# Kernel optimization log

Measured on AMD Instinct MI355X. Metric: run time of the kernel, lower is better.

Reference implementation:

```python
import jax, jax.numpy as jnp
import numpy as np

B, C, H, W = 4, 192, 128, 128
K = 4                       # cross-scan directions (all identical tokens since L=1, but distinct weights)
DSTATE = 8
DTRANK = max(8, C // 16)    # 12
EPS = 1e-5


def _ln(x, w, b):
    mu = jnp.mean(x, axis=-1, keepdims=True)
    var = jnp.var(x, axis=-1, keepdims=True)
    return (x - mu) * jax.lax.rsqrt(var + EPS) * w + b


def setup_inputs() -> dict:
    key = jax.random.key(0)
    ks = jax.random.split(key, 16)
    s_in = 1.0 / np.sqrt(C)
    inp = {
        "x": jax.random.normal(ks[0], (B, C, H, W), jnp.float32),
        "norm_w": 1.0 + 0.02 * jax.random.normal(ks[1], (C,), jnp.float32),
        "norm_b": 0.02 * jax.random.normal(ks[2], (C,), jnp.float32),
        "w_in": s_in * jax.random.normal(ks[3], (2 * C, C), jnp.float32),
        "ssm_in_w": s_in * jax.random.normal(ks[4], (2 * C, C), jnp.float32),
        "x_proj_w": s_in * jax.random.normal(ks[5], (K, DTRANK + 2 * DSTATE, C), jnp.float32),
        "dt_w": (1.0 / np.sqrt(DTRANK)) * jax.random.normal(ks[6], (K, C, DTRANK), jnp.float32),
        "dt_b": 0.1 * jax.random.normal(ks[7], (K, C), jnp.float32),
        "A_logs": jnp.log(jnp.broadcast_to(jnp.arange(1, DSTATE + 1, dtype=jnp.float32), (K * C, DSTATE))),
        "Ds": jnp.ones((K * C,), jnp.float32),
        "out_norm_w": 1.0 + 0.02 * jax.random.normal(ks[8], (C,), jnp.float32),
        "out_norm_b": 0.02 * jax.random.normal(ks[9], (C,), jnp.float32),
        "ssm_out_w": s_in * jax.random.normal(ks[10], (C, C), jnp.float32),
        "w_out": s_in * jax.random.normal(ks[11], (C, C), jnp.float32),
    }
    return inp


def reference(x, norm_w, norm_b, w_in, ssm_in_w, x_proj_w, dt_w, dt_b,
              A_logs, Ds, out_norm_w, out_norm_b, ssm_out_w, w_out):
    # (B,C,H,W) -> (B,H,W,C)
    xh = jnp.transpose(x, (0, 2, 3, 1))
    xn = _ln(xh, norm_w, norm_b)
    p = xn @ w_in.T                         # (B,H,W,2C)
    x1, x2 = p[..., :C], p[..., C:]

    # ---- SS2D (v2, d_conv=1) on per-pixel sequences of length 1 ----
    u = x1 @ ssm_in_w.T                     # (B,H,W,2C)
    xss, z = u[..., :C], u[..., C:]
    z = jax.nn.silu(z)
    xss = jax.nn.silu(xss)

    # x_proj per direction: (B,H,W,K,dt_rank+2*d_state)
    xd = jnp.einsum('bhwd,kcd->bhwkc', xss, x_proj_w)
    dtr = xd[..., :DTRANK]
    Bv = xd[..., DTRANK:DTRANK + DSTATE]
    Cv = xd[..., DTRANK + DSTATE:]
    dt = jax.nn.softplus(jnp.einsum('bhwkr,kdr->bhwkd', dtr, dt_w) + dt_b)

    # Selective scan with L=1 and h0=0: h = dt*B*xss; y_k = sum_s C_s*h_s + D*xss
    # => y = xss * sum_k ( (B . C)_k * dt_k + D_k ).  A = -exp(A_logs) never enters (L=1).
    bc = jnp.sum(Bv * Cv, axis=-1)          # (B,H,W,K)
    gain = jnp.sum(bc[..., None] * dt + Ds.reshape(K, C), axis=-2)  # (B,H,W,C)
    y = xss * gain
    y = _ln(y, out_norm_w, out_norm_b)
    y = y * z
    s = y @ ssm_out_w.T                     # SS2D out_proj

    # ---- block gating + out_proj + residual ----
    o = (s * jax.nn.silu(x2)) @ w_out.T
    return x + jnp.transpose(o, (0, 3, 1, 2))
```

## Files before the change

kernel.cpp:

```cpp
#include <hip/hip_runtime.h>
#include <hip/hip_bf16.h>
#include <math.h>


#define CC    192
#define HH    128
#define WW    128
#define NK    4
#define DST   8
#define DTR   12
#define TP    32
#define SP    200
#define NTH   256

typedef __attribute__((ext_vector_type(8))) short bh8;
typedef __attribute__((ext_vector_type(4))) float f4;

#define OFF_WIN    0
#define OFF_SSMIN  73728
#define OFF_XPROJ  147456
#define OFF_SSMOUT 168960
#define OFF_WOUT   205824
#define OFF_DTW    242688
#define WTOT2      267264

__device__ __forceinline__ float bf2f(unsigned short u) {
    union { unsigned int i; float f; } v; v.i = ((unsigned int)u) << 16; return v.f;
}
__device__ __forceinline__ unsigned short f2bf(float f) {
    union { float f; unsigned int i; } v; v.f = f;
    unsigned int r = (v.i + 0x7fffu + ((v.i >> 16) & 1u)) >> 16;
    return (unsigned short)r;
}
#define LOG2E 1.44269504f
#define LN2   0.69314718f
__device__ __forceinline__ float silu_fast(float x) {
    float e = __builtin_amdgcn_exp2f(-LOG2E * x);
    return x * __builtin_amdgcn_rcpf(1.f + e);
}
__device__ __forceinline__ float softplus_fast(float x) {
    float e = __builtin_amdgcn_exp2f(-LOG2E * fabsf(x));
    return fmaxf(x, 0.f) + LN2 * __builtin_amdgcn_logf(1.f + e);
}

extern "C" __global__ void prep_w(const float* __restrict__ w_in,
                                  const float* __restrict__ ssm_in_w,
                                  const float* __restrict__ x_proj_w,
                                  const float* __restrict__ ssm_out_w,
                                  const float* __restrict__ w_out,
                                  const float* __restrict__ dt_w,
                                  const float* __restrict__ dt_b,
                                  const float* __restrict__ Ds,
                                  unsigned short* __restrict__ wb)
{
    int i = blockIdx.x * NTH + threadIdx.x;
    if (i < OFF_DTW) {
        float v;
        if      (i < OFF_XPROJ ) v = (i < OFF_SSMIN) ? w_in[i] : ssm_in_w[i - OFF_SSMIN];
        else if (i < OFF_SSMOUT) v = x_proj_w[i - OFF_XPROJ];
        else if (i < OFF_WOUT  ) v = ssm_out_w[i - OFF_SSMOUT];
        else                     v = w_out[i - OFF_WOUT];
        wb[i] = f2bf(v);
    } else if (i < WTOT2) {
        int j  = i - OFF_DTW;
        int r  = j & 31;
        int kc = j >> 5;
        float v = (r < DTR) ? dt_w[kc * DTR + r]
                            : (r == 31 ? dt_b[kc] : 0.f);
        wb[i] = f2bf(v);
    } else if (i < WTOT2 + CC) {
        int c = i - WTOT2;
        float* dsum = (float*)(wb + WTOT2);
        dsum[c] = Ds[c] + Ds[CC + c] + Ds[2*CC + c] + Ds[3*CC + c];
    }
}

extern "C" __global__ void __launch_bounds__(NTH, 3)
mamba_fused(const float* __restrict__ x,
            const float* __restrict__ norm_w,  const float* __restrict__ norm_b,
            const float* __restrict__ out_norm_w, const float* __restrict__ out_norm_b,
            const unsigned short* __restrict__ wsb,
            float* __restrict__ out)
{
    __shared__ __align__(16) unsigned short sA [TP][SP];
    __shared__ __align__(16) unsigned short sB [TP][SP];
    __shared__ __align__(16) unsigned short sZ [TP][CC];
    __shared__ __align__(16) unsigned short sX2[TP][CC];
    __shared__ float sred [TP][8];
    __shared__ float sred2[TP][8];
    __shared__ float smu[TP];
    __shared__ float srs[TP];
    __shared__ __align__(16) float sbcT[NK][TP];

    const int tid  = threadIdx.x;
    const int lane = tid & 63;
    const int wave = tid >> 6;
    const int frow = lane & 15;
    const int kb   = lane >> 4;
    const int pxb  = kb * 4;

    const int t   = blockIdx.x;
    const int b   = t >> 9;
    const int rem = t & 511;
    const int h   = rem >> 2;
    const int w0g = (rem & 3) * TP;

    const float* dsum = (const float*)(wsb + WTOT2);

    {
        const int px = tid & 31, part = tid >> 5;
        float sum = 0.f, sq = 0.f;
        const size_t base = (((size_t)b * CC) * HH + h) * WW + w0g + px;
        for (int i = 0; i < 24; ++i) {
            int c = part * 24 + i;
            float v = x[base + (size_t)c * (HH * WW)];
            sum += v; sq += v * v;
            sA[px][c] = f2bf(v);
        }
        sred[px][part] = sum; sred2[px][part] = sq;
        __syncthreads();
        if (part == 0) {
            float s = 0.f, q = 0.f;
            for (int j = 0; j < 8; ++j) { s += sred[px][j]; q += sred2[px][j]; }
            float mu  = s * (1.f / CC);
            float var = q * (1.f / CC) - mu * mu;
            smu[px] = mu; srs[px] = rsqrtf(var + 1e-5f);
        }
        __syncthreads();
        const float mu = smu[px], rs = srs[px];
        for (int i = 0; i < 24; ++i) {
            int c = part * 24 + i;
            float v = bf2f(sA[px][c]);
            v = (v - mu) * rs * norm_w[c] + norm_b[c];
            sA[px][c] = f2bf(v);
        }
        __syncthreads();
    }

    auto load_a = [&](const unsigned short* sSrc, bh8 a[2][6]) {
#pragma unroll
        for (int m = 0; m < 2; ++m)
#pragma unroll
            for (int ks = 0; ks < 6; ++ks)
                a[m][ks] = *(const bh8*)(sSrc + (m * 16 + frow) * SP + ks * 32 + kb * 8);
    };
    auto gemm_nt = [&](const bh8 a[2][6], const unsigned short* wB, int n0,
                       f4& acc0, f4& acc1) {
        const unsigned short* wp = wB + (size_t)(n0 + frow) * CC + kb * 8;
#pragma unroll
        for (int ks = 0; ks < 6; ++ks) {
            bh8 bf = *(const bh8*)(wp + ks * 32);
            acc0 = __builtin_amdgcn_mfma_f32_16x16x32_bf16(a[0][ks], bf, acc0, 0, 0, 0);
            acc1 = __builtin_amdgcn_mfma_f32_16x16x32_bf16(a[1][ks], bf, acc1, 0, 0, 0);
        }
    };

    {
        bh8 a[2][6]; load_a(&sA[0][0], a);
        const unsigned short* wB = wsb + OFF_WIN;
        for (int nt = wave; nt < 24; nt += 4) {
            f4 acc0 = {0.f,0.f,0.f,0.f}, acc1 = {0.f,0.f,0.f,0.f};
            gemm_nt(a, wB, nt * 16, acc0, acc1);
            int o = nt * 16 + frow;
            if (o < CC) {
#pragma unroll
                for (int r = 0; r < 4; ++r) {
                    sB[pxb + r][o]      = f2bf(acc0[r]);
                    sB[16 + pxb + r][o] = f2bf(acc1[r]);
                }
            } else {
                int oc = o - CC;
#pragma unroll
                for (int r = 0; r < 4; ++r) {
                    sX2[pxb + r][oc]      = f2bf(silu_fast(acc0[r]));
                    sX2[16 + pxb + r][oc] = f2bf(silu_fast(acc1[r]));
                }
            }
        }
    }
    __syncthreads();

    {
        bh8 a[2][6]; load_a(&sB[0][0], a);
        const unsigned short* wB = wsb + OFF_SSMIN;
        for (int nt = wave; nt < 24; nt += 4) {
            f4 acc0 = {0.f,0.f,0.f,0.f}, acc1 = {0.f,0.f,0.f,0.f};
            gemm_nt(a, wB, nt * 16, acc0, acc1);
            int o = nt * 16 + frow;
            if (o < CC) {
#pragma unroll
                for (int r = 0; r < 4; ++r) {
                    sA[pxb + r][o]      = f2bf(silu_fast(acc0[r]));
                    sA[16 + pxb + r][o] = f2bf(silu_fast(acc1[r]));
                }
            } else {
                int oc = o - CC;
#pragma unroll
                for (int r = 0; r < 4; ++r) {
                    sZ[pxb + r][oc]      = f2bf(silu_fast(acc0[r]));
                    sZ[16 + pxb + r][oc] = f2bf(silu_fast(acc1[r]));
                }
            }
        }
    }
    __syncthreads();

    {
        bh8 a[2][6]; load_a(&sA[0][0], a);
        const unsigned short* wB = wsb + OFF_XPROJ;
        for (int nt = wave; nt < 7; nt += 4) {
            f4 acc0 = {0.f,0.f,0.f,0.f}, acc1 = {0.f,0.f,0.f,0.f};
            gemm_nt(a, wB, nt * 16, acc0, acc1);
            int o = nt * 16 + frow;
#pragma unroll
            for (int r = 0; r < 4; ++r) {
                sB[pxb + r][o]      = f2bf(acc0[r]);
                sB[16 + pxb + r][o] = f2bf(acc1[r]);
            }
        }
    }
    __syncthreads();

    if (tid < TP * NK) {
        int px = tid & 31, k = tid >> 5;
        float a = 0.f;
        for (int s = 0; s < DST; ++s)
            a += bf2f(sB[px][k*28 + DTR + s]) * bf2f(sB[px][k*28 + DTR + DST + s]);
        sbcT[k][px] = a;
    }
    __syncthreads();

    {
        bh8 adt[NK][2];
#pragma unroll
        for (int k = 0; k < NK; ++k)
#pragma unroll
            for (int m = 0; m < 2; ++m) {
                const unsigned short* rp = &sB[m * 16 + frow][k * 28];
                bh8 v;
                if (kb == 0) {
                    ushort4 lo = *(const ushort4*)(rp);
                    ushort4 hi = *(const ushort4*)(rp + 4);
                    v = bh8{(short)lo.x,(short)lo.y,(short)lo.z,(short)lo.w,
                            (short)hi.x,(short)hi.y,(short)hi.z,(short)hi.w};
                } else if (kb == 1) {
                    ushort4 lo = *(const ushort4*)(rp + 8);
                    v = bh8{(short)lo.x,(short)lo.y,(short)lo.z,(short)lo.w,0,0,0,0};
                } else if (kb == 2) {
                    v = bh8{0,0,0,0,0,0,0,0};
                } else {
                    v = bh8{0,0,0,0,0,0,0,(short)0x3F80};
                }
                adt[k][m] = v;
            }
        f4 bc0[NK], bc1[NK];
#pragma unroll
        for (int k = 0; k < NK; ++k) {
            bc0[k] = *(const f4*)(&sbcT[k][pxb]);
            bc1[k] = *(const f4*)(&sbcT[k][16 + pxb]);
        }
        const unsigned short* wDT = wsb + OFF_DTW;
        for (int ct = wave; ct < 12; ct += 4) {
            int c = ct * 16 + frow;
            f4 g0 = {0.f,0.f,0.f,0.f}, g1 = {0.f,0.f,0.f,0.f};
#pragma unroll
            for (int k = 0; k < NK; ++k) {
                bh8 bf = *(const bh8*)(wDT + (((size_t)(k * CC + c)) << 5) + kb * 8);
                f4 d0 = {0.f,0.f,0.f,0.f}, d1 = {0.f,0.f,0.f,0.f};
                d0 = __builtin_amdgcn_mfma_f32_16x16x32_bf16(adt[k][0], bf, d0, 0, 0, 0);
                d1 = __builtin_amdgcn_mfma_f32_16x16x32_bf16(adt[k][1], bf, d1, 0, 0, 0);
#pragma unroll
                for (int r = 0; r < 4; ++r) {
                    g0[r] += bc0[k][r] * softplus_fast(d0[r]);
                    g1[r] += bc1[k][r] * softplus_fast(d1[r]);
                }
            }
            float ds = dsum[c];
#pragma unroll
            for (int r = 0; r < 4; ++r) {
                float y0 = bf2f(sA[pxb + r][c]) * (g0[r] + ds);
                sA[pxb + r][c] = f2bf(y0);
                float y1 = bf2f(sA[16 + pxb + r][c]) * (g1[r] + ds);
                sA[16 + pxb + r][c] = f2bf(y1);
            }
        }
    }
    __syncthreads();

    {
        const int px = tid & 31, part = tid >> 5;
        float sum = 0.f, sq = 0.f;
        for (int i = 0; i < 24; ++i) {
            int c = part * 24 + i;
            float v = bf2f(sA[px][c]);
            sum += v; sq += v * v;
        }
        sred[px][part] = sum; sred2[px][part] = sq;
        __syncthreads();
        if (part == 0) {
            float s = 0.f, q = 0.f;
            for (int j = 0; j < 8; ++j) { s += sred[px][j]; q += sred2[px][j]; }
            float mu  = s * (1.f / CC);
            float var = q * (1.f / CC) - mu * mu;
            smu[px] = mu; srs[px] = rsqrtf(var + 1e-5f);
        }
        __syncthreads();
        const float mu = smu[px], rs = srs[px];
        for (int i = 0; i < 24; ++i) {
            int c = part * 24 + i;
            float v = bf2f(sA[px][c]);
            v = (v - mu) * rs * out_norm_w[c] + out_norm_b[c];
            v *= bf2f(sZ[px][c]);
            sA[px][c] = f2bf(v);
        }
        __syncthreads();
    }

    {
        bh8 a[2][6]; load_a(&sA[0][0], a);
        const unsigned short* wB = wsb + OFF_SSMOUT;
        for (int nt = wave; nt < 12; nt += 4) {
            f4 acc0 = {0.f,0.f,0.f,0.f}, acc1 = {0.f,0.f,0.f,0.f};
            gemm_nt(a, wB, nt * 16, acc0, acc1);
            int o = nt * 16 + frow;
#pragma unroll
            for (int r = 0; r < 4; ++r) {
                sB[pxb + r][o]      = f2bf(acc0[r] * bf2f(sX2[pxb + r][o]));
                sB[16 + pxb + r][o] = f2bf(acc1[r] * bf2f(sX2[16 + pxb + r][o]));
            }
        }
    }
    __syncthreads();

    {
        bh8 a[2][6]; load_a(&sB[0][0], a);
        const unsigned short* wB = wsb + OFF_WOUT;
        for (int nt = wave; nt < 12; nt += 4) {
            f4 acc0 = {0.f,0.f,0.f,0.f}, acc1 = {0.f,0.f,0.f,0.f};
            gemm_nt(a, wB, nt * 16, acc0, acc1);
            int o = nt * 16 + frow;
            const size_t g0 = (((size_t)b * CC + o) * HH + h) * WW + w0g;
#pragma unroll
            for (int r = 0; r < 4; ++r) {
                out[g0 + pxb + r]      = x[g0 + pxb + r]      + acc0[r];
                out[g0 + 16 + pxb + r] = x[g0 + 16 + pxb + r] + acc1[r];
            }
        }
    }
}

extern "C" void kernel_launch(void* const* d_in, const int* in_sizes, int n_in,
                              void* d_out, int out_size, void* d_ws, size_t ws_size,
                              hipStream_t stream) {
    const float* x          = (const float*)d_in[0];
    const float* norm_w     = (const float*)d_in[1];
    const float* norm_b     = (const float*)d_in[2];
    const float* w_in       = (const float*)d_in[3];
    const float* ssm_in_w   = (const float*)d_in[4];
    const float* x_proj_w   = (const float*)d_in[5];
    const float* dt_w       = (const float*)d_in[6];
    const float* dt_b       = (const float*)d_in[7];
    const float* Ds         = (const float*)d_in[9];
    const float* out_norm_w = (const float*)d_in[10];
    const float* out_norm_b = (const float*)d_in[11];
    const float* ssm_out_w  = (const float*)d_in[12];
    const float* w_out      = (const float*)d_in[13];

    unsigned short* wb = (unsigned short*)d_ws;
    int prep_n = WTOT2 + CC;
    prep_w<<<dim3((prep_n + NTH - 1) / NTH), dim3(NTH), 0, stream>>>(
        w_in, ssm_in_w, x_proj_w, ssm_out_w, w_out, dt_w, dt_b, Ds, wb);

    mamba_fused<<<dim3(2048), dim3(NTH), 0, stream>>>(
        x, norm_w, norm_b, out_norm_w, out_norm_b, wb, (float*)d_out);
}
```

Measured before the change: 176.3 us.

## Keep x2 gate in registers, pair MFMA tiles, raise occupancy to 4 blocks

The silu(x2) gate is now packed as bf16 pairs and held in registers across stages instead of in a shared-memory sX2 buffer. This removes about 12 KB of LDS per block, and the launch bound is raised from 3 to 4 blocks per CU to use the freed space. The GEMM loops are unrolled into explicit pairs of 16-wide output tiles so each wave issues four independent MFMA chains per k-step, giving more instruction-level parallelism. Other tweaks: bf16 conversion now uses the HIP intrinsic, and the bc loads are moved inside the dt loop to cut register pressure. The risk is VGPR spilling under the tighter 4-block bound, and the x_proj stage now computes an extra padded tile.

```diff
diff --git a/kernel.cpp b/kernel.cpp
--- a/kernel.cpp
+++ b/kernel.cpp
@@ -24,14 +24,21 @@
 #define OFF_DTW    242688
 #define WTOT2      267264
 
+#define MFMA(va, vb, vc) __builtin_amdgcn_mfma_f32_16x16x32_bf16(va, vb, vc, 0, 0, 0)
+
 __device__ __forceinline__ float bf2f(unsigned short u) {
     union { unsigned int i; float f; } v; v.i = ((unsigned int)u) << 16; return v.f;
 }
 __device__ __forceinline__ unsigned short f2bf(float f) {
-    union { float f; unsigned int i; } v; v.f = f;
-    unsigned int r = (v.i + 0x7fffu + ((v.i >> 16) & 1u)) >> 16;
-    return (unsigned short)r;
-}
+    __hip_bfloat16 h = __float2bfloat16(f);
+    unsigned short u; __builtin_memcpy(&u, &h, 2); return u;
+}
+__device__ __forceinline__ unsigned int pk2(float a, float b) {
+    return (unsigned int)f2bf(a) | ((unsigned int)f2bf(b) << 16);
+}
+__device__ __forceinline__ float lo16(unsigned int u) { return bf2f((unsigned short)(u & 0xffffu)); }
+__device__ __forceinline__ float hi16(unsigned int u) { return bf2f((unsigned short)(u >> 16)); }
+
 #define LOG2E 1.44269504f
 #define LN2   0.69314718f
 __device__ __forceinline__ float silu_fast(float x) {
@@ -75,7 +82,7 @@
     }
 }
 
-extern "C" __global__ void __launch_bounds__(NTH, 3)
+extern "C" __global__ void __launch_bounds__(NTH, 4)
 mamba_fused(const float* __restrict__ x,
             const float* __restrict__ norm_w,  const float* __restrict__ norm_b,
             const float* __restrict__ out_norm_w, const float* __restrict__ out_norm_b,
@@ -85,7 +92,6 @@
     __shared__ __align__(16) unsigned short sA [TP][SP];
     __shared__ __align__(16) unsigned short sB [TP][SP];
     __shared__ __align__(16) unsigned short sZ [TP][CC];
-    __shared__ __align__(16) unsigned short sX2[TP][CC];
     __shared__ float sred [TP][8];
     __shared__ float sred2[TP][8];
     __shared__ float smu[TP];
@@ -106,6 +112,8 @@
     const int w0g = (rem & 3) * TP;
 
     const float* dsum = (const float*)(wsb + WTOT2);
+
+    uint2 x2a0, x2a1, x2a2, x2b0, x2b1, x2b2;
 
     {
         const int px = tid & 31, part = tid >> 5;
@@ -144,38 +152,76 @@
             for (int ks = 0; ks < 6; ++ks)
                 a[m][ks] = *(const bh8*)(sSrc + (m * 16 + frow) * SP + ks * 32 + kb * 8);
     };
-    auto gemm_nt = [&](const bh8 a[2][6], const unsigned short* wB, int n0,
-                       f4& acc0, f4& acc1) {
+    auto gemm_pair = [&](const bh8 a[2][6], const unsigned short* wB, int n0, int n1,
+                         f4& p0, f4& p1, f4& q0, f4& q1) {
+        const unsigned short* wp0 = wB + (size_t)(n0 + frow) * CC + kb * 8;
+        const unsigned short* wp1 = wB + (size_t)(n1 + frow) * CC + kb * 8;
+#pragma unroll
+        for (int ks = 0; ks < 6; ++ks) {
+            bh8 b0 = *(const bh8*)(wp0 + ks * 32);
+            bh8 b1 = *(const bh8*)(wp1 + ks * 32);
+            p0 = MFMA(a[0][ks], b0, p0);
+            p1 = MFMA(a[1][ks], b0, p1);
+            q0 = MFMA(a[0][ks], b1, q0);
+            q1 = MFMA(a[1][ks], b1, q1);
+        }
+    };
+    auto gemm_one = [&](const bh8 a[2][6], const unsigned short* wB, int n0,
+                        f4& p0, f4& p1) {
         const unsigned short* wp = wB + (size_t)(n0 + frow) * CC + kb * 8;
 #pragma unroll
         for (int ks = 0; ks < 6; ++ks) {
             bh8 bf = *(const bh8*)(wp + ks * 32);
-            acc0 = __builtin_amdgcn_mfma_f32_16x16x32_bf16(a[0][ks], bf, acc0, 0, 0, 0);
-            acc1 = __builtin_amdgcn_mfma_f32_16x16x32_bf16(a[1][ks], bf, acc1, 0, 0, 0);
-        }
+            p0 = MFMA(a[0][ks], bf, p0);
+            p1 = MFMA(a[1][ks], bf, p1);
+        }
+    };
+    auto st_sB = [&](int o, const f4& c0, const f4& c1) {
+#pragma unroll
+        for (int r = 0; r < 4; ++r) {
+            sB[pxb + r][o]      = f2bf(c0[r]);
+            sB[16 + pxb + r][o] = f2bf(c1[r]);
+        }
+    };
+    auto st_sA_silu = [&](int o, const f4& c0, const f4& c1) {
+#pragma unroll
+        for (int r = 0; r < 4; ++r) {
+            sA[pxb + r][o]      = f2bf(silu_fast(c0[r]));
+            sA[16 + pxb + r][o] = f2bf(silu_fast(c1[r]));
+        }
+    };
+    auto st_sZ_silu = [&](int oc, const f4& c0, const f4& c1) {
+#pragma unroll
+        for (int r = 0; r < 4; ++r) {
+            sZ[pxb + r][oc]      = f2bf(silu_fast(c0[r]));
+            sZ[16 + pxb + r][oc] = f2bf(silu_fast(c1[r]));
+        }
+    };
+    auto pack_silu = [&](const f4& c) {
+        return make_uint2(pk2(silu_fast(c[0]), silu_fast(c[1])),
+                          pk2(silu_fast(c[2]), silu_fast(c[3])));
     };
 
     {
         bh8 a[2][6]; load_a(&sA[0][0], a);
         const unsigned short* wB = wsb + OFF_WIN;
-        for (int nt = wave; nt < 24; nt += 4) {
-            f4 acc0 = {0.f,0.f,0.f,0.f}, acc1 = {0.f,0.f,0.f,0.f};
-            gemm_nt(a, wB, nt * 16, acc0, acc1);
-            int o = nt * 16 + frow;
-            if (o < CC) {
-#pragma unroll
-                for (int r = 0; r < 4; ++r) {
-                    sB[pxb + r][o]      = f2bf(acc0[r]);
-                    sB[16 + pxb + r][o] = f2bf(acc1[r]);
-                }
-            } else {
-                int oc = o - CC;
-#pragma unroll
-                for (int r = 0; r < 4; ++r) {
-                    sX2[pxb + r][oc]      = f2bf(silu_fast(acc0[r]));
-                    sX2[16 + pxb + r][oc] = f2bf(silu_fast(acc1[r]));
-                }
-            }
+        {
+            f4 p0={0,0,0,0},p1={0,0,0,0},q0={0,0,0,0},q1={0,0,0,0};
+            gemm_pair(a, wB, wave * 16, (wave + 4) * 16, p0, p1, q0, q1);
+            st_sB(wave * 16 + frow, p0, p1);
+            st_sB((wave + 4) * 16 + frow, q0, q1);
+        }
+        {
+            f4 p0={0,0,0,0},p1={0,0,0,0},q0={0,0,0,0},q1={0,0,0,0};
+            gemm_pair(a, wB, (wave + 8) * 16, (wave + 12) * 16, p0, p1, q0, q1);
+            st_sB((wave + 8) * 16 + frow, p0, p1);
+            x2a0 = pack_silu(q0); x2b0 = pack_silu(q1);
+        }
+        {
+            f4 p0={0,0,0,0},p1={0,0,0,0},q0={0,0,0,0},q1={0,0,0,0};
+            gemm_pair(a, wB, (wave + 16) * 16, (wave + 20) * 16, p0, p1, q0, q1);
+            x2a1 = pack_silu(p0); x2b1 = pack_silu(p1);
+            x2a2 = pack_silu(q0); x2b2 = pack_silu(q1);
         }
     }
     __syncthreads();
@@ -183,24 +229,23 @@
     {
         bh8 a[2][6]; load_a(&sB[0][0], a);
         const unsigned short* wB = wsb + OFF_SSMIN;
-        for (int nt = wave; nt < 24; nt += 4) {
-            f4 acc0 = {0.f,0.f,0.f,0.f}, acc1 = {0.f,0.f,0.f,0.f};
-            gemm_nt(a, wB, nt * 16, acc0, acc1);
-            int o = nt * 16 + frow;
-            if (o < CC) {
-#pragma unroll
-                for (int r = 0; r < 4; ++r) {
-                    sA[pxb + r][o]      = f2bf(silu_fast(acc0[r]));
-                    sA[16 + pxb + r][o] = f2bf(silu_fast(acc1[r]));
-                }
-            } else {
-                int oc = o - CC;
-#pragma unroll
-                for (int r = 0; r < 4; ++r) {
-                    sZ[pxb + r][oc]      = f2bf(silu_fast(acc0[r]));
-                    sZ[16 + pxb + r][oc] = f2bf(silu_fast(acc1[r]));
-                }
-            }
+        {
+            f4 p0={0,0,0,0},p1={0,0,0,0},q0={0,0,0,0},q1={0,0,0,0};
+            gemm_pair(a, wB, wave * 16, (wave + 4) * 16, p0, p1, q0, q1);
+            st_sA_silu(wave * 16 + frow, p0, p1);
+            st_sA_silu((wave + 4) * 16 + frow, q0, q1);
+        }
+        {
+            f4 p0={0,0,0,0},p1={0,0,0,0},q0={0,0,0,0},q1={0,0,0,0};
+            gemm_pair(a, wB, (wave + 8) * 16, (wave + 12) * 16, p0, p1, q0, q1);
+            st_sA_silu((wave + 8) * 16 + frow, p0, p1);
+            st_sZ_silu((wave + 12) * 16 + frow - CC, q0, q1);
+        }
+        {
+            f4 p0={0,0,0,0},p1={0,0,0,0},q0={0,0,0,0},q1={0,0,0,0};
+            gemm_pair(a, wB, (wave + 16) * 16, (wave + 20) * 16, p0, p1, q0, q1);
+            st_sZ_silu((wave + 16) * 16 + frow - CC, p0, p1);
+            st_sZ_silu((wave + 20) * 16 + frow - CC, q0, q1);
         }
     }
     __syncthreads();
@@ -208,16 +253,10 @@
     {
         bh8 a[2][6]; load_a(&sA[0][0], a);
         const unsigned short* wB = wsb + OFF_XPROJ;
-        for (int nt = wave; nt < 7; nt += 4) {
-            f4 acc0 = {0.f,0.f,0.f,0.f}, acc1 = {0.f,0.f,0.f,0.f};
-            gemm_nt(a, wB, nt * 16, acc0, acc1);
-            int o = nt * 16 + frow;
-#pragma unroll
-            for (int r = 0; r < 4; ++r) {
-                sB[pxb + r][o]      = f2bf(acc0[r]);
-                sB[16 + pxb + r][o] = f2bf(acc1[r]);
-            }
-        }
+        f4 p0={0,0,0,0},p1={0,0,0,0},q0={0,0,0,0},q1={0,0,0,0};
+        gemm_pair(a, wB, wave * 16, (wave + 4) * 16, p0, p1, q0, q1);
+        st_sB(wave * 16 + frow, p0, p1);
+        st_sB((wave + 4) * 16 + frow, q0, q1);
     }
     __syncthreads();
 
@@ -253,12 +292,6 @@
                 }
                 adt[k][m] = v;
             }
-        f4 bc0[NK], bc1[NK];
-#pragma unroll
-        for (int k = 0; k < NK; ++k) {
-            bc0[k] = *(const f4*)(&sbcT[k][pxb]);
-            bc1[k] = *(const f4*)(&sbcT[k][16 + pxb]);
-        }
         const unsigned short* wDT = wsb + OFF_DTW;
         for (int ct = wave; ct < 12; ct += 4) {
             int c = ct * 16 + frow;
@@ -267,12 +300,14 @@
             for (int k = 0; k < NK; ++k) {
                 bh8 bf = *(const bh8*)(wDT + (((size_t)(k * CC + c)) << 5) + kb * 8);
                 f4 d0 = {0.f,0.f,0.f,0.f}, d1 = {0.f,0.f,0.f,0.f};
-                d0 = __builtin_amdgcn_mfma_f32_16x16x32_bf16(adt[k][0], bf, d0, 0, 0, 0);
-                d1 = __builtin_amdgcn_mfma_f32_16x16x32_bf16(adt[k][1], bf, d1, 0, 0, 0);
+                d0 = MFMA(adt[k][0], bf, d0);
+                d1 = MFMA(adt[k][1], bf, d1);
+                f4 bc0 = *(const f4*)(&sbcT[k][pxb]);
+                f4 bc1 = *(const f4*)(&sbcT[k][16 + pxb]);
 #pragma unroll
                 for (int r = 0; r < 4; ++r) {
-                    g0[r] += bc0[k][r] * softplus_fast(d0[r]);
-                    g1[r] += bc1[k][r] * softplus_fast(d1[r]);
+                    g0[r] += bc0[r] * softplus_fast(d0[r]);
+                    g1[r] += bc1[r] * softplus_fast(d1[r]);
                 }
             }
             float ds = dsum[c];
@@ -319,15 +354,39 @@
     {
         bh8 a[2][6]; load_a(&sA[0][0], a);
         const unsigned short* wB = wsb + OFF_SSMOUT;
-        for (int nt = wave; nt < 12; nt += 4) {
-            f4 acc0 = {0.f,0.f,0.f,0.f}, acc1 = {0.f,0.f,0.f,0.f};
-            gemm_nt(a, wB, nt * 16, acc0, acc1);
-            int o = nt * 16 + frow;
-#pragma unroll
-            for (int r = 0; r < 4; ++r) {
-                sB[pxb + r][o]      = f2bf(acc0[r] * bf2f(sX2[pxb + r][o]));
-                sB[16 + pxb + r][o] = f2bf(acc1[r] * bf2f(sX2[16 + pxb + r][o]));
-            }
+        {
+            f4 p0={0,0,0,0},p1={0,0,0,0},q0={0,0,0,0},q1={0,0,0,0};
+            gemm_pair(a, wB, wave * 16, (wave + 4) * 16, p0, p1, q0, q1);
+            int o0 = wave * 16 + frow, o1 = (wave + 4) * 16 + frow;
+            sB[pxb + 0][o0]      = f2bf(p0[0] * lo16(x2a0.x));
+            sB[pxb + 1][o0]      = f2bf(p0[1] * hi16(x2a0.x));
+            sB[pxb + 2][o0]      = f2bf(p0[2] * lo16(x2a0.y));
+            sB[pxb + 3][o0]      = f2bf(p0[3] * hi16(x2a0.y));
+            sB[16 + pxb + 0][o0] = f2bf(p1[0] * lo16(x2b0.x));
+            sB[16 + pxb + 1][o0] = f2bf(p1[1] * hi16(x2b0.x));
+            sB[16 + pxb + 2][o0] = f2bf(p1[2] * lo16(x2b0.y));
+            sB[16 + pxb + 3][o0] = f2bf(p1[3] * hi16(x2b0.y));
+            sB[pxb + 0][o1]      = f2bf(q0[0] * lo16(x2a1.x));
+            sB[pxb + 1][o1]      = f2bf(q0[1] * hi16(x2a1.x));
+            sB[pxb + 2][o1]      = f2bf(q0[2] * lo16(x2a1.y));
+            sB[pxb + 3][o1]      = f2bf(q0[3] * hi16(x2a1.y));
+            sB[16 + pxb + 0][o1] = f2bf(q1[0] * lo16(x2b1.x));
+            sB[16 + pxb + 1][o1] = f2bf(q1[1] * hi16(x2b1.x));
+            sB[16 + pxb + 2][o1] = f2bf(q1[2] * lo16(x2b1.y));
+            sB[16 + pxb + 3][o1] = f2bf(q1[3] * hi16(x2b1.y));
+        }
+        {
+            f4 p0={0,0,0,0},p1={0,0,0,0};
+            gemm_one(a, wB, (wave + 8) * 16, p0, p1);
+            int o = (wave + 8) * 16 + frow;
+            sB[pxb + 0][o]      = f2bf(p0[0] * lo16(x2a2.x));
+            sB[pxb + 1][o]      = f2bf(p0[1] * hi16(x2a2.x));
+            sB[pxb + 2][o]      = f2bf(p0[2] * lo16(x2a2.y));
+            sB[pxb + 3][o]      = f2bf(p0[3] * hi16(x2a2.y));
+            sB[16 + pxb + 0][o] = f2bf(p1[0] * lo16(x2b2.x));
+            sB[16 + pxb + 1][o] = f2bf(p1[1] * hi16(x2b2.x));
+            sB[16 + pxb + 2][o] = f2bf(p1[2] * lo16(x2b2.y));
+            sB[16 + pxb + 3][o] = f2bf(p1[3] * hi16(x2b2.y));
         }
     }
     __syncthreads();
@@ -335,16 +394,24 @@
     {
         bh8 a[2][6]; load_a(&sB[0][0], a);
         const unsigned short* wB = wsb + OFF_WOUT;
-        for (int nt = wave; nt < 12; nt += 4) {
-            f4 acc0 = {0.f,0.f,0.f,0.f}, acc1 = {0.f,0.f,0.f,0.f};
-            gemm_nt(a, wB, nt * 16, acc0, acc1);
-            int o = nt * 16 + frow;
+        auto st_out = [&](int o, const f4& c0, const f4& c1) {
             const size_t g0 = (((size_t)b * CC + o) * HH + h) * WW + w0g;
 #pragma unroll
             for (int r = 0; r < 4; ++r) {
-                out[g0 + pxb + r]      = x[g0 + pxb + r]      + acc0[r];
-                out[g0 + 16 + pxb + r] = x[g0 + 16 + pxb + r] + acc1[r];
+                out[g0 + pxb + r]      = x[g0 + pxb + r]      + c0[r];
+                out[g0 + 16 + pxb + r] = x[g0 + 16 + pxb + r] + c1[r];
             }
+        };
+        {
+            f4 p0={0,0,0,0},p1={0,0,0,0},q0={0,0,0,0},q1={0,0,0,0};
+            gemm_pair(a, wB, wave * 16, (wave + 4) * 16, p0, p1, q0, q1);
+            st_out(wave * 16 + frow, p0, p1);
+            st_out((wave + 4) * 16 + frow, q0, q1);
+        }
+        {
+            f4 p0={0,0,0,0},p1={0,0,0,0};
+            gemm_one(a, wB, (wave + 8) * 16, p0, p1);
+            st_out((wave + 8) * 16 + frow, p0, p1);
         }
     }
 }
```

Measured after the change: 152.6 us. 13.5% less time.

## Make each wave own 16 pixels end-to-end with register-held intermediates and no block syncs

Applied to the files above, without the earlier changes.

The kernel changes from a block that shares 32 pixels across 4 waves, with many __syncthreads between GEMM stages, to one where each wave processes its own 16 pixels through every stage. Per-wave shared-memory slices, shuffle-based LayerNorm reductions and packed bf16 register storage for x2, z and y remove the block barriers and cut shared-memory use, and launch bounds rise to 4 blocks per SM. Each wave now reads the full weight matrices for only 16 pixels, which halves weight reuse per MFMA and raises L2 weight traffic. Register pressure also goes up from the 48-float input array and the packed arrays.

```diff
diff --git a/kernel.cpp b/kernel.cpp
--- a/kernel.cpp
+++ b/kernel.cpp
@@ -9,9 +9,9 @@
 #define NK    4
 #define DST   8
 #define DTR   12
-#define TP    32
+#define NTH   256
 #define SP    200
-#define NTH   256
+#define SD    112
 
 typedef __attribute__((ext_vector_type(8))) short bh8;
 typedef __attribute__((ext_vector_type(4))) float f4;
@@ -24,14 +24,21 @@
 #define OFF_DTW    242688
 #define WTOT2      267264
 
+#define MFMA(va, vb, vc) __builtin_amdgcn_mfma_f32_16x16x32_bf16(va, vb, vc, 0, 0, 0)
+
 __device__ __forceinline__ float bf2f(unsigned short u) {
     union { unsigned int i; float f; } v; v.i = ((unsigned int)u) << 16; return v.f;
 }
 __device__ __forceinline__ unsigned short f2bf(float f) {
-    union { float f; unsigned int i; } v; v.f = f;
-    unsigned int r = (v.i + 0x7fffu + ((v.i >> 16) & 1u)) >> 16;
-    return (unsigned short)r;
-}
+    __hip_bfloat16 h = __float2bfloat16(f);
+    unsigned short u; __builtin_memcpy(&u, &h, 2); return u;
+}
+__device__ __forceinline__ unsigned int pk2(float a, float b) {
+    return (unsigned int)f2bf(a) | ((unsigned int)f2bf(b) << 16);
+}
+__device__ __forceinline__ float lo16(unsigned int u) { return bf2f((unsigned short)(u & 0xffffu)); }
+__device__ __forceinline__ float hi16(unsigned int u) { return bf2f((unsigned short)(u >> 16)); }
+
 #define LOG2E 1.44269504f
 #define LN2   0.69314718f
 __device__ __forceinline__ float silu_fast(float x) {
@@ -75,275 +82,284 @@
     }
 }
 
-extern "C" __global__ void __launch_bounds__(NTH, 3)
+template<int NT>
+__device__ __forceinline__ void gemmN(const bh8 a[6], const unsigned short* wp,
+                                      f4 acc[NT]) {
+#pragma unroll
+    for (int ks = 0; ks < 6; ++ks)
+#pragma unroll
+        for (int j = 0; j < NT; ++j) {
+            bh8 bf = *(const bh8*)(wp + (size_t)j * 16 * CC + ks * 32);
+            acc[j] = MFMA(a[ks], bf, acc[j]);
+        }
+}
+
+extern "C" __global__ void __launch_bounds__(NTH, 4)
 mamba_fused(const float* __restrict__ x,
             const float* __restrict__ norm_w,  const float* __restrict__ norm_b,
             const float* __restrict__ out_norm_w, const float* __restrict__ out_norm_b,
             const unsigned short* __restrict__ wsb,
             float* __restrict__ out)
 {
-    __shared__ __align__(16) unsigned short sA [TP][SP];
-    __shared__ __align__(16) unsigned short sB [TP][SP];
-    __shared__ __align__(16) unsigned short sZ [TP][CC];
-    __shared__ __align__(16) unsigned short sX2[TP][CC];
-    __shared__ float sred [TP][8];
-    __shared__ float sred2[TP][8];
-    __shared__ float smu[TP];
-    __shared__ float srs[TP];
-    __shared__ __align__(16) float sbcT[NK][TP];
+    __shared__ __align__(16) unsigned short sX [4][16][SP];
+    __shared__ __align__(16) unsigned short sXD[4][16][SD];
+    __shared__ __align__(16) float sbc[4][NK][16];
 
     const int tid  = threadIdx.x;
     const int lane = tid & 63;
-    const int wave = tid >> 6;
+    const int wv   = tid >> 6;
     const int frow = lane & 15;
     const int kb   = lane >> 4;
     const int pxb  = kb * 4;
 
     const int t   = blockIdx.x;
-    const int b   = t >> 9;
-    const int rem = t & 511;
-    const int h   = rem >> 2;
-    const int w0g = (rem & 3) * TP;
+    const int b   = t >> 8;
+    const int rem = t & 255;
+    const int h   = rem >> 1;
+    const int w0  = (rem & 1) * 64 + wv * 16;
+
+    unsigned short (*mX)[SP]  = sX[wv];
+    unsigned short (*mXD)[SD] = sXD[wv];
+    float (*mbc)[16]          = sbc[wv];
 
     const float* dsum = (const float*)(wsb + WTOT2);
 
-    {
-        const int px = tid & 31, part = tid >> 5;
+    unsigned int x2p[12][2], zp[12][2];
+
+    {
+        const int c0 = kb * 48;
+        const size_t base = (((size_t)b * CC + c0) * HH + h) * WW + w0 + frow;
+        float v[48];
         float sum = 0.f, sq = 0.f;
-        const size_t base = (((size_t)b * CC) * HH + h) * WW + w0g + px;
-        for (int i = 0; i < 24; ++i) {
-            int c = part * 24 + i;
-            float v = x[base + (size_t)c * (HH * WW)];
-            sum += v; sq += v * v;
-            sA[px][c] = f2bf(v);
-        }
-        sred[px][part] = sum; sred2[px][part] = sq;
-        __syncthreads();
-        if (part == 0) {
-            float s = 0.f, q = 0.f;
-            for (int j = 0; j < 8; ++j) { s += sred[px][j]; q += sred2[px][j]; }
-            float mu  = s * (1.f / CC);
-            float var = q * (1.f / CC) - mu * mu;
-            smu[px] = mu; srs[px] = rsqrtf(var + 1e-5f);
-        }
-        __syncthreads();
-        const float mu = smu[px], rs = srs[px];
-        for (int i = 0; i < 24; ++i) {
-            int c = part * 24 + i;
-            float v = bf2f(sA[px][c]);
-            v = (v - mu) * rs * norm_w[c] + norm_b[c];
-            sA[px][c] = f2bf(v);
-        }
-        __syncthreads();
-    }
-
-    auto load_a = [&](const unsigned short* sSrc, bh8 a[2][6]) {
-#pragma unroll
-        for (int m = 0; m < 2; ++m)
-#pragma unroll
-            for (int ks = 0; ks < 6; ++ks)
-                a[m][ks] = *(const bh8*)(sSrc + (m * 16 + frow) * SP + ks * 32 + kb * 8);
+#pragma unroll
+        for (int i = 0; i < 48; ++i) {
+            v[i] = x[base + (size_t)i * (HH * WW)];
+            sum += v[i]; sq += v[i] * v[i];
+        }
+        sum += __shfl_xor(sum, 16); sum += __shfl_xor(sum, 32);
+        sq  += __shfl_xor(sq , 16); sq  += __shfl_xor(sq , 32);
+        float mu = sum * (1.f / CC);
+        float rs = rsqrtf(sq * (1.f / CC) - mu * mu + 1e-5f);
+#pragma unroll
+        for (int i = 0; i < 48; ++i) {
+            int c = c0 + i;
+            mX[frow][c] = f2bf((v[i] - mu) * rs * norm_w[c] + norm_b[c]);
+        }
+    }
+
+    bh8 a[6];
+    auto load_a = [&]() {
+#pragma unroll
+        for (int ks = 0; ks < 6; ++ks)
+            a[ks] = *(const bh8*)(&mX[frow][ks * 32 + kb * 8]);
     };
-    auto gemm_nt = [&](const bh8 a[2][6], const unsigned short* wB, int n0,
-                       f4& acc0, f4& acc1) {
-        const unsigned short* wp = wB + (size_t)(n0 + frow) * CC + kb * 8;
-#pragma unroll
-        for (int ks = 0; ks < 6; ++ks) {
-            bh8 bf = *(const bh8*)(wp + ks * 32);
-            acc0 = __builtin_amdgcn_mfma_f32_16x16x32_bf16(a[0][ks], bf, acc0, 0, 0, 0);
-            acc1 = __builtin_amdgcn_mfma_f32_16x16x32_bf16(a[1][ks], bf, acc1, 0, 0, 0);
-        }
-    };
-
-    {
-        bh8 a[2][6]; load_a(&sA[0][0], a);
+
+    {
+        load_a();
         const unsigned short* wB = wsb + OFF_WIN;
-        for (int nt = wave; nt < 24; nt += 4) {
-            f4 acc0 = {0.f,0.f,0.f,0.f}, acc1 = {0.f,0.f,0.f,0.f};
-            gemm_nt(a, wB, nt * 16, acc0, acc1);
-            int o = nt * 16 + frow;
-            if (o < CC) {
-#pragma unroll
-                for (int r = 0; r < 4; ++r) {
-                    sB[pxb + r][o]      = f2bf(acc0[r]);
-                    sB[16 + pxb + r][o] = f2bf(acc1[r]);
+#pragma unroll
+        for (int g = 0; g < 6; ++g) {
+            f4 acc[4] = {{0,0,0,0},{0,0,0,0},{0,0,0,0},{0,0,0,0}};
+            gemmN<4>(a, wB + (size_t)(g * 64 + frow) * CC + kb * 8, acc);
+#pragma unroll
+            for (int j = 0; j < 4; ++j) {
+                int tile = g * 4 + j;
+                int o = tile * 16 + frow;
+                if (tile < 12) {
+#pragma unroll
+                    for (int r = 0; r < 4; ++r) mX[pxb + r][o] = f2bf(acc[j][r]);
+                } else {
+                    x2p[tile - 12][0] = pk2(silu_fast(acc[j][0]), silu_fast(acc[j][1]));
+                    x2p[tile - 12][1] = pk2(silu_fast(acc[j][2]), silu_fast(acc[j][3]));
                 }
+            }
+        }
+    }
+
+    {
+        load_a();
+        const unsigned short* wB = wsb + OFF_SSMIN;
+#pragma unroll
+        for (int g = 0; g < 6; ++g) {
+            f4 acc[4] = {{0,0,0,0},{0,0,0,0},{0,0,0,0},{0,0,0,0}};
+            gemmN<4>(a, wB + (size_t)(g * 64 + frow) * CC + kb * 8, acc);
+#pragma unroll
+            for (int j = 0; j < 4; ++j) {
+                int tile = g * 4 + j;
+                int o = tile * 16 + frow;
+                if (tile < 12) {
+#pragma unroll
+                    for (int r = 0; r < 4; ++r)
+                        mX[pxb + r][o] = f2bf(silu_fast(acc[j][r]));
+                } else {
+                    zp[tile - 12][0] = pk2(silu_fast(acc[j][0]), silu_fast(acc[j][1]));
+                    zp[tile - 12][1] = pk2(silu_fast(acc[j][2]), silu_fast(acc[j][3]));
+                }
+            }
+        }
+    }
+
+    {
+        load_a();
+        const unsigned short* wB = wsb + OFF_XPROJ;
+        {
+            f4 acc[4] = {{0,0,0,0},{0,0,0,0},{0,0,0,0},{0,0,0,0}};
+            gemmN<4>(a, wB + (size_t)frow * CC + kb * 8, acc);
+#pragma unroll
+            for (int j = 0; j < 4; ++j) {
+                int o = j * 16 + frow;
+#pragma unroll
+                for (int r = 0; r < 4; ++r) mXD[pxb + r][o] = f2bf(acc[j][r]);
+            }
+        }
+        {
+            f4 acc[3] = {{0,0,0,0},{0,0,0,0},{0,0,0,0}};
+            gemmN<3>(a, wB + (size_t)(64 + frow) * CC + kb * 8, acc);
+#pragma unroll
+            for (int j = 0; j < 3; ++j) {
+                int o = (4 + j) * 16 + frow;
+#pragma unroll
+                for (int r = 0; r < 4; ++r) mXD[pxb + r][o] = f2bf(acc[j][r]);
+            }
+        }
+    }
+
+    {
+        const unsigned short* rp = &mXD[frow][kb * 28 + DTR];
+        float acc = 0.f;
+#pragma unroll
+        for (int s = 0; s < DST; ++s)
+            acc += bf2f(rp[s]) * bf2f(rp[DST + s]);
+        mbc[kb][frow] = acc;
+    }
+
+    unsigned int yp[12][2];
+    {
+        bh8 adt[NK];
+#pragma unroll
+        for (int k = 0; k < NK; ++k) {
+            const unsigned short* rp = &mXD[frow][k * 28];
+            bh8 vv;
+            if (kb == 0) {
+                ushort4 lo = *(const ushort4*)(rp);
+                ushort4 hi = *(const ushort4*)(rp + 4);
+                vv = bh8{(short)lo.x,(short)lo.y,(short)lo.z,(short)lo.w,
+                         (short)hi.x,(short)hi.y,(short)hi.z,(short)hi.w};
+            } else if (kb == 1) {
+                ushort4 lo = *(const ushort4*)(rp + 8);
+                vv = bh8{(short)lo.x,(short)lo.y,(short)lo.z,(short)lo.w,0,0,0,0};
+            } else if (kb == 2) {
+                vv = bh8{0,0,0,0,0,0,0,0};
             } else {
-                int oc = o - CC;
-#pragma unroll
-                for (int r = 0; r < 4; ++r) {
-                    sX2[pxb + r][oc]      = f2bf(silu_fast(acc0[r]));
-                    sX2[16 + pxb + r][oc] = f2bf(silu_fast(acc1[r]));
-                }
-            }
-        }
-    }
-    __syncthreads();
-
-    {
-        bh8 a[2][6]; load_a(&sB[0][0], a);
-        const unsigned short* wB = wsb + OFF_SSMIN;
-        for (int nt = wave; nt < 24; nt += 4) {
-            f4 acc0 = {0.f,0.f,0.f,0.f}, acc1 = {0.f,0.f,0.f,0.f};
-            gemm_nt(a, wB, nt * 16, acc0, acc1);
-            int o = nt * 16 + frow;
-            if (o < CC) {
-#pragma unroll
-                for (int r = 0; r < 4; ++r) {
-                    sA[pxb + r][o]      = f2bf(silu_fast(acc0[r]));
-                    sA[16 + pxb + r][o] = f2bf(silu_fast(acc1[r]));
-                }
-            } else {
-                int oc = o - CC;
-#pragma unroll
-                for (int r = 0; r < 4; ++r) {
-                    sZ[pxb + r][oc]      = f2bf(silu_fast(acc0[r]));
-                    sZ[16 + pxb + r][oc] = f2bf(silu_fast(acc1[r]));
-                }
-            }
-        }
-    }
-    __syncthreads();
-
-    {
-        bh8 a[2][6]; load_a(&sA[0][0], a);
-        const unsigned short* wB = wsb + OFF_XPROJ;
-        for (int nt = wave; nt < 7; nt += 4) {
-            f4 acc0 = {0.f,0.f,0.f,0.f}, acc1 = {0.f,0.f,0.f,0.f};
-            gemm_nt(a, wB, nt * 16, acc0, acc1);
-            int o = nt * 16 + frow;
-#pragma unroll
-            for (int r = 0; r < 4; ++r) {
-                sB[pxb + r][o]      = f2bf(acc0[r]);
-                sB[16 + pxb + r][o] = f2bf(acc1[r]);
-            }
-        }
-    }
-    __syncthreads();
-
-    if (tid < TP * NK) {
-        int px = tid & 31, k = tid >> 5;
-        float a = 0.f;
-        for (int s = 0; s < DST; ++s)
-            a += bf2f(sB[px][k*28 + DTR + s]) * bf2f(sB[px][k*28 + DTR + DST + s]);
-        sbcT[k][px] = a;
-    }
-    __syncthreads();
-
-    {
-        bh8 adt[NK][2];
-#pragma unroll
-        for (int k = 0; k < NK; ++k)
-#pragma unroll
-            for (int m = 0; m < 2; ++m) {
-                const unsigned short* rp = &sB[m * 16 + frow][k * 28];
-                bh8 v;
-                if (kb == 0) {
-                    ushort4 lo = *(const ushort4*)(rp);
-                    ushort4 hi = *(const ushort4*)(rp + 4);
-                    v = bh8{(short)lo.x,(short)lo.y,(short)lo.z,(short)lo.w,
-                            (short)hi.x,(short)hi.y,(short)hi.z,(short)hi.w};
-                } else if (kb == 1) {
-                    ushort4 lo = *(const ushort4*)(rp + 8);
-                    v = bh8{(short)lo.x,(short)lo.y,(short)lo.z,(short)lo.w,0,0,0,0};
-                } else if (kb == 2) {
-                    v = bh8{0,0,0,0,0,0,0,0};
-                } else {
-                    v = bh8{0,0,0,0,0,0,0,(short)0x3F80};
-                }
-                adt[k][m] = v;
-            }
-        f4 bc0[NK], bc1[NK];
-#pragma unroll
-        for (int k = 0; k < NK; ++k) {
-            bc0[k] = *(const f4*)(&sbcT[k][pxb]);
-            bc1[k] = *(const f4*)(&sbcT[k][16 + pxb]);
-        }
+                vv = bh8{0,0,0,0,0,0,0,(short)0x3F80};
+            }
+            adt[k] = vv;
+        }
+        f4 bck[NK];
+#pragma unroll
+        for (int k = 0; k < NK; ++k) bck[k] = *(const f4*)(&mbc[k][pxb]);
+
         const unsigned short* wDT = wsb + OFF_DTW;
-        for (int ct = wave; ct < 12; ct += 4) {
+#pragma unroll
+        for (int ct = 0; ct < 12; ++ct) {
             int c = ct * 16 + frow;
-            f4 g0 = {0.f,0.f,0.f,0.f}, g1 = {0.f,0.f,0.f,0.f};
+            f4 g = {0.f,0.f,0.f,0.f};
 #pragma unroll
             for (int k = 0; k < NK; ++k) {
                 bh8 bf = *(const bh8*)(wDT + (((size_t)(k * CC + c)) << 5) + kb * 8);
-                f4 d0 = {0.f,0.f,0.f,0.f}, d1 = {0.f,0.f,0.f,0.f};
-                d0 = __builtin_amdgcn_mfma_f32_16x16x32_bf16(adt[k][0], bf, d0, 0, 0, 0);
-                d1 = __builtin_amdgcn_mfma_f32_16x16x32_bf16(adt[k][1], bf, d1, 0, 0, 0);
-#pragma unroll
-                for (int r = 0; r < 4; ++r) {
-                    g0[r] += bc0[k][r] * softplus_fast(d0[r]);
-                    g1[r] += bc1[k][r] * softplus_fast(d1[r]);
-                }
+                f4 d = {0.f,0.f,0.f,0.f};
+                d = MFMA(adt[k], bf, d);
+#pragma unroll
+                for (int r = 0; r < 4; ++r)
+                    g[r] += bck[k][r] * softplus_fast(d[r]);
             }
             float ds = dsum[c];
+            float y0 = bf2f(mX[pxb + 0][c]) * (g[0] + ds);
+            float y1 = bf2f(mX[pxb + 1][c]) * (g[1] + ds);
+            float y2 = bf2f(mX[pxb + 2][c]) * (g[2] + ds);
+            float y3 = bf2f(mX[pxb + 3][c]) * (g[3] + ds);
+            yp[ct][0] = pk2(y0, y1);
+            yp[ct][1] = pk2(y2, y3);
+        }
+    }
+
+    {
+        f4 sum = {0,0,0,0}, sq = {0,0,0,0};
+#pragma unroll
+        for (int ct = 0; ct < 12; ++ct) {
+            float y0 = lo16(yp[ct][0]), y1 = hi16(yp[ct][0]);
+            float y2 = lo16(yp[ct][1]), y3 = hi16(yp[ct][1]);
+            sum[0] += y0; sq[0] += y0 * y0;
+            sum[1] += y1; sq[1] += y1 * y1;
+            sum[2] += y2; sq[2] += y2 * y2;
+            sum[3] += y3; sq[3] += y3 * y3;
+        }
+#pragma unroll
+        for (int m = 1; m < 16; m <<= 1) {
 #pragma unroll
             for (int r = 0; r < 4; ++r) {
-                float y0 = bf2f(sA[pxb + r][c]) * (g0[r] + ds);
-                sA[pxb + r][c] = f2bf(y0);
-                float y1 = bf2f(sA[16 + pxb + r][c]) * (g1[r] + ds);
-                sA[16 + pxb + r][c] = f2bf(y1);
-            }
-        }
-    }
-    __syncthreads();
-
-    {
-        const int px = tid & 31, part = tid >> 5;
-        float sum = 0.f, sq = 0.f;
-        for (int i = 0; i < 24; ++i) {
-            int c = part * 24 + i;
-            float v = bf2f(sA[px][c]);
-            sum += v; sq += v * v;
-        }
-        sred[px][part] = sum; sred2[px][part] = sq;
-        __syncthreads();
-        if (part == 0) {
-            float s = 0.f, q = 0.f;
-            for (int j = 0; j < 8; ++j) { s += sred[px][j]; q += sred2[px][j]; }
-            float mu  = s * (1.f / CC);
-            float var = q * (1.f / CC) - mu * mu;
-            smu[px] = mu; srs[px] = rsqrtf(var + 1e-5f);
-        }
-        __syncthreads();
-        const float mu = smu[px], rs = srs[px];
-        for (int i = 0; i < 24; ++i) {
-            int c = part * 24 + i;
-            float v = bf2f(sA[px][c]);
-            v = (v - mu) * rs * out_norm_w[c] + out_norm_b[c];
-            v *= bf2f(sZ[px][c]);
-            sA[px][c] = f2bf(v);
-        }
-        __syncthreads();
-    }
-
-    {
-        bh8 a[2][6]; load_a(&sA[0][0], a);
+                sum[r] += __shfl_xor(sum[r], m);
+                sq[r]  += __shfl_xor(sq[r],  m);
+            }
+        }
+        f4 mu, rs;
+#pragma unroll
+        for (int r = 0; r < 4; ++r) {
+            mu[r] = sum[r] * (1.f / CC);
+            rs[r] = rsqrtf(sq[r] * (1.f / CC) - mu[r] * mu[r] + 1e-5f);
+        }
+#pragma unroll
+        for (int ct = 0; ct < 12; ++ct) {
+            int c = ct * 16 + frow;
+            float wn = out_norm_w[c], bn = out_norm_b[c];
+            float y0 = lo16(yp[ct][0]), y1 = hi16(yp[ct][0]);
+            float y2 = lo16(yp[ct][1]), y3 = hi16(yp[ct][1]);
+            float z0 = lo16(zp[ct][0]), z1 = hi16(zp[ct][0]);
+            float z2 = lo16(zp[ct][1]), z3 = hi16(zp[ct][1]);
+            mX[pxb + 0][c] = f2bf(((y0 - mu[0]) * rs[0] * wn + bn) * z0);
+            mX[pxb + 1][c] = f2bf(((y1 - mu[1]) * rs[1] * wn + bn) * z1);
+            mX[pxb + 2][c] = f2bf(((y2 - mu[2]) * rs[2] * wn + bn) * z2);
+            mX[pxb + 3][c] = f2bf(((y3 - mu[3]) * rs[3] * wn + bn) * z3);
+        }
+    }
+
+    {
+        load_a();
         const unsigned short* wB = wsb + OFF_SSMOUT;
-        for (int nt = wave; nt < 12; nt += 4) {
-            f4 acc0 = {0.f,0.f,0.f,0.f}, acc1 = {0.f,0.f,0.f,0.f};
-            gemm_nt(a, wB, nt * 16, acc0, acc1);
-            int o = nt * 16 + frow;
-#pragma unroll
-            for (int r = 0; r < 4; ++r) {
-                sB[pxb + r][o]      = f2bf(acc0[r] * bf2f(sX2[pxb + r][o]));
-                sB[16 + pxb + r][o] = f2bf(acc1[r] * bf2f(sX2[16 + pxb + r][o]));
-            }
-        }
-    }
-    __syncthreads();
-
-    {
-        bh8 a[2][6]; load_a(&sB[0][0], a);
+#pragma unroll
+        for (int g = 0; g < 3; ++g) {
+            f4 acc[4] = {{0,0,0,0},{0,0,0,0},{0,0,0,0},{0,0,0,0}};
+            gemmN<4>(a, wB + (size_t)(g * 64 + frow) * CC + kb * 8, acc);
+#pragma unroll
+            for (int j = 0; j < 4; ++j) {
+                int tile = g * 4 + j;
+                int o = tile * 16 + frow;
+                mX[pxb + 0][o] = f2bf(acc[j][0] * lo16(x2p[tile][0]));
+                mX[pxb + 1][o] = f2bf(acc[j][1] * hi16(x2p[tile][0]));
+                mX[pxb + 2][o] = f2bf(acc[j][2] * lo16(x2p[tile][1]));
+                mX[pxb + 3][o] = f2bf(acc[j][3] * hi16(x2p[tile][1]));
+            }
+        }
+    }
+
+    {
+        load_a();
         const unsigned short* wB = wsb + OFF_WOUT;
-        for (int nt = wave; nt < 12; nt += 4) {
-            f4 acc0 = {0.f,0.f,0.f,0.f}, acc1 = {0.f,0.f,0.f,0.f};
-            gemm_nt(a, wB, nt * 16, acc0, acc1);
-            int o = nt * 16 + frow;
-            const size_t g0 = (((size_t)b * CC + o) * HH + h) * WW + w0g;
-#pragma unroll
-            for (int r = 0; r < 4; ++r) {
-                out[g0 + pxb + r]      = x[g0 + pxb + r]      + acc0[r];
-                out[g0 + 16 + pxb + r] = x[g0 + 16 + pxb + r] + acc1[r];
+#pragma unroll
+        for (int g = 0; g < 3; ++g) {
+            f4 acc[4] = {{0,0,0,0},{0,0,0,0},{0,0,0,0},{0,0,0,0}};
+            gemmN<4>(a, wB + (size_t)(g * 64 + frow) * CC + kb * 8, acc);
+#pragma unroll
+            for (int j = 0; j < 4; ++j) {
+                int o = (g * 4 + j) * 16 + frow;
+                const size_t g0 = (((size_t)b * CC + o) * HH + h) * WW + w0 + pxb;
+                float4 xv = *(const float4*)(x + g0);
+                float4 ov;
+                ov.x = xv.x + acc[j][0];
+                ov.y = xv.y + acc[j][1];
+                ov.z = xv.z + acc[j][2];
+                ov.w = xv.w + acc[j][3];
+                *(float4*)(out + g0) = ov;
             }
         }
     }
@@ -371,6 +387,6 @@
     prep_w<<<dim3((prep_n + NTH - 1) / NTH), dim3(NTH), 0, stream>>>(
         w_in, ssm_in_w, x_proj_w, ssm_out_w, w_out, dt_w, dt_b, Ds, wb);
 
-    mamba_fused<<<dim3(2048), dim3(NTH), 0, stream>>>(
+    mamba_fused<<<dim3(1024), dim3(NTH), 0, stream>>>(
         x, norm_w, norm_b, out_norm_w, out_norm_b, wb, (float*)d_out);
 }
```

Result: slower. 368.2 us (+108.8%).
